# Performance work log

Hardware: AMD Instinct MI355X
Metric: run time of the kernel (lower is better)

The kernel has to match this reference:

```python
import jax, jax.numpy as jnp
import numpy as np

B, H, W, N = 4, 64, 64, 64
NEAR, FAR = 2.0, 6.0
HID = 64


def setup_inputs() -> dict:
    key = jax.random.key(0)
    ks = jax.random.split(key, 6)
    ray_origins = jnp.tile(jnp.array([0.0, 0.0, 4.0], jnp.float32), (B, H, W, 1))
    ray_directions = jax.random.normal(ks[0], (B, H, W, 3), jnp.float32)
    tform_cam2world = jnp.eye(4, dtype=jnp.float32) + 0.1 * jax.random.normal(ks[1], (B, 4, 4), jnp.float32)
    depth_noise = jax.random.uniform(ks[2], (B, H, W, N), jnp.float32)
    u_samples = jax.random.uniform(ks[3], (B, H, W, N), jnp.float32)
    W1 = 0.5 * jax.random.normal(ks[4], (3, HID), jnp.float32)
    b1 = jnp.zeros((HID,), jnp.float32)
    W2 = 0.5 * jax.random.normal(ks[5], (HID, 4), jnp.float32)
    b2 = jnp.zeros((4,), jnp.float32)
    return dict(ray_origins=ray_origins, ray_directions=ray_directions,
                tform_cam2world=tform_cam2world, depth_noise=depth_noise,
                u_samples=u_samples, W1=W1, b1=b1, W2=W2, b2=b2)


def field(pts, W1, b1, W2, b2):
    # tiny radiance-field MLP standing in for the generator's sampler
    h = jax.nn.relu(pts @ W1 + b1)
    out = h @ W2 + b2
    sigma = out[..., 0]
    rgb = jax.nn.sigmoid(out[..., 1:4])
    return sigma, rgb


def compositing_weights(sigma, z_vals):
    # alpha-compositing weights (render_volume_density)
    dists = jnp.concatenate([z_vals[..., 1:] - z_vals[..., :-1],
                             jnp.full_like(z_vals[..., :1], 1e10)], axis=-1)
    alpha = 1.0 - jnp.exp(-jax.nn.relu(sigma) * dists)
    trans = jnp.cumprod(1.0 - alpha + 1e-10, axis=-1)
    trans = jnp.concatenate([jnp.ones_like(trans[..., :1]), trans[..., :-1]], axis=-1)
    return alpha * trans


def sample_pdf(bins, weights, u):
    # bins [R, M+1], weights [R, M], u [R, S] -> samples [R, S]
    pdf = weights / jnp.sum(weights, axis=-1, keepdims=True)
    cdf = jnp.cumsum(pdf, axis=-1)
    cdf = jnp.concatenate([jnp.zeros_like(cdf[..., :1]), cdf], axis=-1)  # [R, M+1]
    inds = jax.vmap(lambda c, uu: jnp.searchsorted(c, uu, side='right'))(cdf, u)
    last = cdf.shape[-1] - 1
    below = jnp.clip(inds - 1, 0, last)
    above = jnp.clip(inds, 0, last)
    cdf_b = jnp.take_along_axis(cdf, below, axis=-1)
    cdf_a = jnp.take_along_axis(cdf, above, axis=-1)
    bin_b = jnp.take_along_axis(bins, below, axis=-1)
    bin_a = jnp.take_along_axis(bins, above, axis=-1)
    denom = cdf_a - cdf_b
    denom = jnp.where(denom < 1e-5, 1.0, denom)
    t = (u - cdf_b) / denom
    return bin_b + t * (bin_a - bin_b)


def reference(ray_origins, ray_directions, tform_cam2world, depth_noise, u_samples, W1, b1, W2, b2):
    rd = ray_directions / jnp.linalg.norm(ray_directions, axis=-1, keepdims=True)
    # stratified coarse samples along each ray
    t = (jnp.arange(N, dtype=jnp.float32) + depth_noise) / N           # [B,H,W,N]
    z_vals = NEAR + (FAR - NEAR) * t
    pts = ray_origins[..., None, :] + rd[..., None, :] * z_vals[..., None]
    sigma, rgb = field(pts, W1, b1, W2, b2)                            # [B,H,W,N], [B,H,W,N,3]

    # --- hierarchical importance sampling (no_grad in original) ---
    w = compositing_weights(sigma, z_vals).reshape(-1, N)              # [R,N]
    pad = jnp.pad(w, ((0, 0), (1, 1)), constant_values=-jnp.inf)
    mx = jnp.maximum(pad[:, :-1], pad[:, 1:])                          # max_pool1d(k=2,s=1,p=1) -> [R,N+1]
    sm = 0.5 * (mx[:, :-1] + mx[:, 1:]) + 0.01                        # avg_pool1d(k=2,s=1)  -> [R,N]
    z_mid = (0.5 * (z_vals[..., 1:] + z_vals[..., :-1])).reshape(-1, N - 1)
    z_samples = sample_pdf(z_mid, sm[:, 1:-1], u_samples.reshape(-1, N))
    z_samples = jax.lax.stop_gradient(z_samples.reshape(B, H, W, N))

    # fine evaluation + merge-sort of coarse/fine samples
    z_all = jnp.concatenate([z_vals, z_samples], axis=-1)              # [B,H,W,2N]
    idx = jnp.argsort(z_all, axis=-1)
    z_sorted = jnp.take_along_axis(z_all, idx, axis=-1)
    pts_f = ray_origins[..., None, :] + rd[..., None, :] * z_samples[..., None]
    sigma_f, rgb_f = field(pts_f, W1, b1, W2, b2)
    sigma_all = jnp.take_along_axis(jnp.concatenate([sigma, sigma_f], axis=-1), idx, axis=-1)
    rgb_cat = jnp.concatenate([rgb, rgb_f], axis=-2)
    rgb_all = jnp.take_along_axis(rgb_cat, jnp.broadcast_to(idx[..., None], idx.shape + (3,)), axis=-2)

    # final alpha compositing
    w_all = compositing_weights(sigma_all, z_sorted)
    rgb_pred = jnp.sum(w_all[..., None] * rgb_all, axis=-2)            # [B,H,W,3]
    depth_pred = jnp.sum(w_all * z_sorted, axis=-1)                    # [B,H,W]
    mask_pred = jnp.sum(w_all, axis=-1)                                # [B,H,W]

    # camera-space depth (invert_space: R_w2c = R^T)
    R_w2c = jnp.swapaxes(tform_cam2world[:, :3, :3], -1, -2)           # [B,3,3]
    view_dir = jnp.einsum('bhwj,bij->bhwi', rd, R_w2c)
    depth_cam = -(view_dir * depth_pred[..., None])[..., -1]
    return rgb_pred, depth_cam, mask_pred
```

## Files before the change

### kernel.cpp

```cpp
#include <hip/hip_runtime.h>
#include <hip/hip_bf16.h>
#include <math.h>

#define Nn    64
#define RPB   2
#define NRAYS 16384
#define NEARV 2.0f
#define FARV  6.0f

typedef __attribute__((ext_vector_type(8))) short bf16x8;
typedef __attribute__((ext_vector_type(4))) float f32x4;
typedef __attribute__((ext_vector_type(2))) float f32x2;

template <int CTRL, int RMASK>
__device__ __forceinline__ float dpp_mv(float x, float ident) {
  return __int_as_float(__builtin_amdgcn_update_dpp(
      __float_as_int(ident), __float_as_int(x), CTRL, RMASK, 0xf, false));
}
__device__ __forceinline__ float shfl_up1(float x) {
  return __int_as_float(__builtin_amdgcn_update_dpp(
      __float_as_int(x), __float_as_int(x), 0x138, 0xf, 0xf, false));
}
__device__ __forceinline__ float shfl_dn1(float x) {
  return __int_as_float(__builtin_amdgcn_update_dpp(
      __float_as_int(x), __float_as_int(x), 0x130, 0xf, 0xf, false));
}
__device__ __forceinline__ float scan_add_dpp(float x) {
  x += dpp_mv<0x111, 0xf>(x, 0.f);
  x += dpp_mv<0x112, 0xf>(x, 0.f);
  x += dpp_mv<0x114, 0xf>(x, 0.f);
  x += dpp_mv<0x118, 0xf>(x, 0.f);
  x += dpp_mv<0x142, 0xa>(x, 0.f);
  x += dpp_mv<0x143, 0xc>(x, 0.f);
  return x;
}
__device__ __forceinline__ float scan_mul_dpp(float x) {
  x *= dpp_mv<0x111, 0xf>(x, 1.f);
  x *= dpp_mv<0x112, 0xf>(x, 1.f);
  x *= dpp_mv<0x114, 0xf>(x, 1.f);
  x *= dpp_mv<0x118, 0xf>(x, 1.f);
  x *= dpp_mv<0x142, 0xa>(x, 1.f);
  x *= dpp_mv<0x143, 0xc>(x, 1.f);
  return x;
}
__device__ __forceinline__ float reduce_add_bcast(float x) {
  x = scan_add_dpp(x);
  return __int_as_float(__builtin_amdgcn_readlane(__float_as_int(x), 63));
}

__device__ __forceinline__ float fast_rcp(float x) { return __builtin_amdgcn_rcpf(x); }
__device__ __forceinline__ float sigmoidf_fast(float x) { return fast_rcp(1.f + __expf(-x)); }

__device__ __forceinline__ short bfhi_bits(float x) { return (short)(__float_as_uint(x) >> 16); }
__device__ __forceinline__ float bfhi_val(float x)  { return __uint_as_float(__float_as_uint(x) & 0xFFFF0000u); }

template <int LEVEL, int D>
__device__ __forceinline__ void bitonic_stage(unsigned& k, int lane) {
  unsigned t;
  if constexpr (D == 32) {
    t = (unsigned)__builtin_amdgcn_ds_bpermute((lane ^ 32) << 2, (int)k);
  } else {
    t = (unsigned)__builtin_amdgcn_ds_swizzle((int)k, (D << 10) | 0x1F);
  }
  const bool bitd = (lane & D) != 0;
  const bool desc = (lane & (1 << LEVEL)) != 0;
  const unsigned mn = (k < t) ? k : t;
  const unsigned mx = (k < t) ? t : k;
  k = (bitd == desc) ? mn : mx;
}
template <int LEVEL, int D>
struct BSort {
  static __device__ __forceinline__ void run(unsigned& k, int lane) {
    bitonic_stage<LEVEL, D>(k, lane);
    if constexpr (D > 1) BSort<LEVEL, D / 2>::run(k, lane);
    else if constexpr (LEVEL < 6) BSort<LEVEL + 1, (1 << LEVEL)>::run(k, lane);
  }
};

template <int D>
__device__ __forceinline__ void merge_stage(unsigned& k, int lane) {
  unsigned t;
  if constexpr (D == 32) {
    t = (unsigned)__builtin_amdgcn_ds_bpermute((lane ^ 32) << 2, (int)k);
  } else {
    t = (unsigned)__builtin_amdgcn_ds_swizzle((int)k, (D << 10) | 0x1F);
  }
  const unsigned mn = (k < t) ? k : t;
  const unsigned mx = (k < t) ? t : k;
  k = ((lane & D) != 0) ? mx : mn;
}
__device__ __forceinline__ void merge64(unsigned& k, int lane) {
  merge_stage<32>(k, lane);
  merge_stage<16>(k, lane);
  merge_stage<8>(k, lane);
  merge_stage<4>(k, lane);
  merge_stage<2>(k, lane);
  merge_stage<1>(k, lane);
}

__device__ __forceinline__ int count_le_f(float arr, float x) {
  int cnt = 0;
#pragma unroll
  for (int step = 32; step >= 1; step >>= 1) {
    const int idx = cnt + step - 1;
    const float v = __shfl(arr, idx, 64);
    if (idx < 63 && v <= x) cnt += step;
  }
  return cnt;
}

template <bool SPLITB>
__device__ __forceinline__ void field_eval(
    float zlane, const f32x2 c0v[2][4], const f32x2 c1v[2][4],
    const bf16x8 aHi[2], const bf16x8 aLo[2],
    float b20, float b21, float b22, float b23,
    int quad, int col, float4* scratch, float o[4]) {
#pragma unroll
  for (int nt = 0; nt < 4; ++nt) {
    f32x4 acc = {0.f, 0.f, 0.f, 0.f};
    const float zm = __shfl(zlane, nt * 16 + col, 64);
    const f32x2 zm2 = {zm, zm};
#pragma unroll
    for (int ks = 0; ks < 2; ++ks) {
      union { bf16x8 v; unsigned u[4]; } Bhi, Blo;
#pragma unroll
      for (int p = 0; p < 4; ++p) {
        f32x2 h = zm2 * c1v[ks][p] + c0v[ks][p];
        h = __builtin_elementwise_max(h, (f32x2){0.f, 0.f});
        if constexpr (SPLITB) {
          union { f32x2 f; unsigned u[2]; } U; U.f = h;
          Bhi.u[p] = __builtin_amdgcn_perm(U.u[1], U.u[0], 0x07060302u);
          union { unsigned u[2]; f32x2 f; } M;
          M.u[0] = U.u[0] & 0xFFFF0000u;
          M.u[1] = U.u[1] & 0xFFFF0000u;
          const f32x2 l = h - M.f;
          union { f32x2 f; unsigned u[2]; } L; L.f = l;
          Blo.u[p] = __builtin_amdgcn_perm(L.u[1], L.u[0], 0x07060302u);
        } else {
          __hip_bfloat162 t = __float22bfloat162_rn(make_float2(h[0], h[1]));
          Bhi.u[p] = *reinterpret_cast<unsigned*>(&t);
        }
      }
      if constexpr (SPLITB) {
        acc = __builtin_amdgcn_mfma_f32_16x16x32_bf16(aHi[ks], Bhi.v, acc, 0, 0, 0);
        acc = __builtin_amdgcn_mfma_f32_16x16x32_bf16(aHi[ks], Blo.v, acc, 0, 0, 0);
        acc = __builtin_amdgcn_mfma_f32_16x16x32_bf16(aLo[ks], Bhi.v, acc, 0, 0, 0);
      } else {
        acc = __builtin_amdgcn_mfma_f32_16x16x32_bf16(aHi[ks], Bhi.v, acc, 0, 0, 0);
        acc = __builtin_amdgcn_mfma_f32_16x16x32_bf16(aLo[ks], Bhi.v, acc, 0, 0, 0);
      }
    }
    if (quad == 0) scratch[nt * 16 + col] = make_float4(acc[0], acc[1], acc[2], acc[3]);
  }
  const float4 r = scratch[(threadIdx.x & 63)];
  o[0] = r.x + b20; o[1] = r.y + b21; o[2] = r.z + b22; o[3] = r.w + b23;
}

__global__ __launch_bounds__(RPB * 64, 4) void nerf_fused(
    const float* __restrict__ ray_o, const float* __restrict__ ray_d,
    const float* __restrict__ tform, const float* __restrict__ noise,
    const float* __restrict__ usmp,  const float* __restrict__ W1,
    const float* __restrict__ b1,    const float* __restrict__ W2,
    const float* __restrict__ b2,    float* __restrict__ out) {
  const int wave = threadIdx.x >> 6;
  const int lane = threadIdx.x & 63;
  const int ray  = blockIdx.x * RPB + wave;
  const int quad = lane >> 4;
  const int col  = lane & 15;

  __shared__ float2 sC [RPB][Nn];
  __shared__ float4 sPk[RPB][2 * Nn];

  const float o0 = ray_o[ray * 3 + 0], o1 = ray_o[ray * 3 + 1], o2 = ray_o[ray * 3 + 2];
  float d0 = ray_d[ray * 3 + 0], d1 = ray_d[ray * 3 + 1], d2 = ray_d[ray * 3 + 2];
  const float rn = __builtin_amdgcn_rsqf(d0 * d0 + d1 * d1 + d2 * d2);
  d0 *= rn; d1 *= rn; d2 *= rn;

  {
    const float w10 = W1[lane], w11 = W1[64 + lane], w12 = W1[128 + lane];
    const float c1 = d0 * w10 + d1 * w11 + d2 * w12;
    const float c0 = o0 * w10 + o1 * w11 + o2 * w12 + b1[lane];
    sC[wave][lane] = make_float2(c0, c1);
  }

  const float nz = noise[ray * Nn + lane];
  const float z  = NEARV + (FARV - NEARV) * ((float)lane + nz) * (1.0f / Nn);
  const unsigned kc = ((__float_as_uint(z) - 0x40000000u) << 7) | (unsigned)lane;

  f32x2 c0v[2][4], c1v[2][4];
#pragma unroll
  for (int ks = 0; ks < 2; ++ks) {
    const float4* cc4 = (const float4*)&sC[wave][0];
    const int base4 = (ks * 32 + quad * 8) >> 1;
#pragma unroll
    for (int jj = 0; jj < 4; ++jj) {
      const float4 v = cc4[base4 + jj];
      c0v[ks][jj] = (f32x2){v.x, v.z};
      c1v[ks][jj] = (f32x2){v.y, v.w};
    }
  }

  bf16x8 aHi[2], aLo[2];
#pragma unroll
  for (int ks = 0; ks < 2; ++ks) {
#pragma unroll
    for (int j = 0; j < 8; ++j) {
      const int k = ks * 32 + quad * 8 + j;
      const float wv  = (col < 4) ? W2[k * 4 + col] : 0.f;
      aHi[ks][j] = bfhi_bits(wv);
      aLo[ks][j] = bfhi_bits(wv - bfhi_val(wv));
    }
  }
  const float b20 = b2[0], b21 = b2[1], b22 = b2[2], b23 = b2[3];
  float4* scratch = &sPk[wave][64];

  float oc[4];
  field_eval<true>(z, c0v, c1v, aHi, aLo, b20, b21, b22, b23, quad, col, scratch, oc);
  const float sig = oc[0];
  const float cr = sigmoidf_fast(oc[1]), cg = sigmoidf_fast(oc[2]), cb = sigmoidf_fast(oc[3]);
  sPk[wave][lane] = make_float4(sig, cr, cg, cb);

  const float zn   = shfl_dn1(z);
  const float dist = (lane == 63) ? 1e10f : (zn - z);
  const float alpha = 1.f - __expf(-fmaxf(sig, 0.f) * dist);
  float cdfreg, binreg;
  {
    const float P  = scan_mul_dpp(1.f - alpha + 1e-10f);
    float Te = shfl_up1(P);
    if (lane == 0) Te = 1.f;
    const float w = alpha * Te;

    const float mxA = fmaxf(shfl_up1(w), w);
    const float mxB = fmaxf(w, shfl_dn1(w));
    const float sm = 0.5f * (mxA + mxB) + 0.01f;

    const float v   = (lane >= 1 && lane <= 62) ? sm : 0.f;
    const float tot = reduce_add_bcast(v);
    const float pdf = v * fast_rcp(tot);
    const float C   = scan_add_dpp(pdf);
    cdfreg = (lane == 0) ? 0.f : C;
    binreg = 0.5f * (z + zn);
  }

  const float u = usmp[ray * Nn + lane];
  const int lo_i = count_le_f(cdfreg, u);
  const int below = lo_i - 1;
  const int above = (lo_i < 63) ? lo_i : 62;
  const float cdfb = __shfl(cdfreg, below, 64);
  const float cdfa = __shfl(cdfreg, above, 64);
  const float binb = __shfl(binreg, below, 64);
  const float bina = __shfl(binreg, above, 64);
  float den = cdfa - cdfb;
  if (den < 1e-5f) den = 1.f;
  const float zs = fmaf((u - cdfb) * fast_rcp(den), bina - binb, binb);

  const unsigned kf = ((__float_as_uint(zs) - 0x40000000u) << 7) | (unsigned)(64 + lane);
  unsigned kfS = kf;
  BSort<1, 1>::run(kfS, lane);

  float of[4];
  field_eval<false>(zs, c0v, c1v, aHi, aLo, b20, b21, b22, b23, quad, col, scratch, of);

  unsigned lok = kc;
  unsigned hik = (unsigned)__builtin_amdgcn_ds_bpermute((63 - lane) << 2, (int)kfS);
  {
    const unsigned mn = (lok < hik) ? lok : hik;
    const unsigned mx = (lok < hik) ? hik : lok;
    lok = mn; hik = mx;
  }
  merge64(lok, lane);
  merge64(hik, lane);

  const float sigF = of[0];
  const float fr = sigmoidf_fast(of[1]), fg = sigmoidf_fast(of[2]), fb = sigmoidf_fast(of[3]);
  sPk[wave][64 + lane] = make_float4(sigF, fr, fg, fb);

  const int a0 = ((2 * lane) & 63) << 2;
  const int a1 = ((2 * lane + 1) & 63) << 2;
  const unsigned l0 = (unsigned)__builtin_amdgcn_ds_bpermute(a0, (int)lok);
  const unsigned h0 = (unsigned)__builtin_amdgcn_ds_bpermute(a0, (int)hik);
  const unsigned l1 = (unsigned)__builtin_amdgcn_ds_bpermute(a1, (int)lok);
  const unsigned h1 = (unsigned)__builtin_amdgcn_ds_bpermute(a1, (int)hik);
  const unsigned k0 = (lane < 32) ? l0 : h0;
  const unsigned k1 = (lane < 32) ? l1 : h1;

  const float z0 = __uint_as_float((k0 >> 7) + 0x40000000u);
  const float z1 = __uint_as_float((k1 >> 7) + 0x40000000u);
  const float4 q0 = sPk[wave][k0 & 127u];
  const float4 q1 = sPk[wave][k1 & 127u];

  const float z2 = shfl_dn1(z0);
  const float dist0 = z1 - z0;
  const float dist1 = (lane == 63) ? 1e10f : (z2 - z1);
  const float al0 = 1.f - __expf(-fmaxf(q0.x, 0.f) * dist0);
  const float al1 = 1.f - __expf(-fmaxf(q1.x, 0.f) * dist1);
  const float aa0 = 1.f - al0 + 1e-10f;
  const float aa1 = 1.f - al1 + 1e-10f;
  const float Pp = scan_mul_dpp(aa0 * aa1);
  float Tp = shfl_up1(Pp);
  if (lane == 0) Tp = 1.f;
  const float w0 = al0 * Tp;
  const float w1 = al1 * Tp * aa0;

  const float accR = reduce_add_bcast(w0 * q0.y + w1 * q1.y);
  const float accG = reduce_add_bcast(w0 * q0.z + w1 * q1.z);
  const float accB = reduce_add_bcast(w0 * q0.w + w1 * q1.w);
  const float accD = reduce_add_bcast(w0 * z0 + w1 * z1);
  const float accM = reduce_add_bcast(w0 + w1);

  if (lane == 0) {
    const float* tf = tform + (ray >> 12) * 16;
    const float vz = d0 * tf[2] + d1 * tf[6] + d2 * tf[10];
    out[ray * 3 + 0]     = accR;
    out[ray * 3 + 1]     = accG;
    out[ray * 3 + 2]     = accB;
    out[NRAYS * 3 + ray] = -vz * accD;
    out[NRAYS * 4 + ray] = accM;
  }
}

extern "C" void kernel_launch(void* const* d_in, const int* in_sizes, int n_in,
                              void* d_out, int out_size, void* d_ws, size_t ws_size,
                              hipStream_t stream) {
  const float* ray_o = (const float*)d_in[0];
  const float* ray_d = (const float*)d_in[1];
  const float* tform = (const float*)d_in[2];
  const float* noise = (const float*)d_in[3];
  const float* usmp  = (const float*)d_in[4];
  const float* W1    = (const float*)d_in[5];
  const float* b1    = (const float*)d_in[6];
  const float* W2    = (const float*)d_in[7];
  const float* b2    = (const float*)d_in[8];
  float* out = (float*)d_out;

  nerf_fused<<<dim3(NRAYS / RPB), RPB * 64, 0, stream>>>(
      ray_o, ray_d, tform, noise, usmp, W1, b1, W2, b2, out);
}
```

Baseline: 101.8 us.

## Process two rays per wavefront to interleave independent dependency chains

Each wave now handles two rays, with per-ray state in arrays and each stage (field eval, scans, sampling, sort/merge, compositing) run for both rays back to back. This gives the scheduler independent instructions to hide latency in the serial DPP scans, shuffles and MFMA chains, and reuses W1/W2 register loads across rays. The grid is halved and launch bounds drop to 2 waves/SIMD, so register pressure and occupancy shift in exchange for ILP.

```diff
diff --git a/kernel.cpp b/kernel.cpp
--- a/kernel.cpp
+++ b/kernel.cpp
@@ -3,7 +3,7 @@
 #include <math.h>
 
 #define Nn    64
-#define RPB   2
+#define WPB   2
 #define NRAYS 16384
 #define NEARV 2.0f
 #define FARV  6.0f
@@ -156,7 +156,7 @@
   o[0] = r.x + b20; o[1] = r.y + b21; o[2] = r.z + b22; o[3] = r.w + b23;
 }
 
-__global__ __launch_bounds__(RPB * 64, 4) void nerf_fused(
+__global__ __launch_bounds__(WPB * 64, 2) void nerf_fused(
     const float* __restrict__ ray_o, const float* __restrict__ ray_d,
     const float* __restrict__ tform, const float* __restrict__ noise,
     const float* __restrict__ usmp,  const float* __restrict__ W1,
@@ -164,39 +164,47 @@
     const float* __restrict__ b2,    float* __restrict__ out) {
   const int wave = threadIdx.x >> 6;
   const int lane = threadIdx.x & 63;
-  const int ray  = blockIdx.x * RPB + wave;
+  const int ray0 = (blockIdx.x * WPB + wave) * 2;
   const int quad = lane >> 4;
   const int col  = lane & 15;
 
-  __shared__ float2 sC [RPB][Nn];
-  __shared__ float4 sPk[RPB][2 * Nn];
-
-  const float o0 = ray_o[ray * 3 + 0], o1 = ray_o[ray * 3 + 1], o2 = ray_o[ray * 3 + 2];
-  float d0 = ray_d[ray * 3 + 0], d1 = ray_d[ray * 3 + 1], d2 = ray_d[ray * 3 + 2];
-  const float rn = __builtin_amdgcn_rsqf(d0 * d0 + d1 * d1 + d2 * d2);
-  d0 *= rn; d1 *= rn; d2 *= rn;
-
-  {
-    const float w10 = W1[lane], w11 = W1[64 + lane], w12 = W1[128 + lane];
-    const float c1 = d0 * w10 + d1 * w11 + d2 * w12;
-    const float c0 = o0 * w10 + o1 * w11 + o2 * w12 + b1[lane];
-    sC[wave][lane] = make_float2(c0, c1);
-  }
-
-  const float nz = noise[ray * Nn + lane];
-  const float z  = NEARV + (FARV - NEARV) * ((float)lane + nz) * (1.0f / Nn);
-  const unsigned kc = ((__float_as_uint(z) - 0x40000000u) << 7) | (unsigned)lane;
-
-  f32x2 c0v[2][4], c1v[2][4];
-#pragma unroll
-  for (int ks = 0; ks < 2; ++ks) {
-    const float4* cc4 = (const float4*)&sC[wave][0];
-    const int base4 = (ks * 32 + quad * 8) >> 1;
-#pragma unroll
-    for (int jj = 0; jj < 4; ++jj) {
-      const float4 v = cc4[base4 + jj];
-      c0v[ks][jj] = (f32x2){v.x, v.z};
-      c1v[ks][jj] = (f32x2){v.y, v.w};
+  __shared__ float2 sC [WPB][2][Nn];
+  __shared__ float4 sPk[WPB][2][2 * Nn];
+
+  const float w10 = W1[lane], w11 = W1[64 + lane], w12 = W1[128 + lane];
+  const float b1v = b1[lane];
+
+  float d0[2], d1[2], d2[2], z[2];
+  unsigned kc[2];
+#pragma unroll
+  for (int r = 0; r < 2; ++r) {
+    const int ray = ray0 + r;
+    const float o0 = ray_o[ray * 3 + 0], o1 = ray_o[ray * 3 + 1], o2 = ray_o[ray * 3 + 2];
+    float dd0 = ray_d[ray * 3 + 0], dd1 = ray_d[ray * 3 + 1], dd2 = ray_d[ray * 3 + 2];
+    const float rn = __builtin_amdgcn_rsqf(dd0 * dd0 + dd1 * dd1 + dd2 * dd2);
+    dd0 *= rn; dd1 *= rn; dd2 *= rn;
+    d0[r] = dd0; d1[r] = dd1; d2[r] = dd2;
+    const float c1 = dd0 * w10 + dd1 * w11 + dd2 * w12;
+    const float c0 = o0 * w10 + o1 * w11 + o2 * w12 + b1v;
+    sC[wave][r][lane] = make_float2(c0, c1);
+    const float nz = noise[ray * Nn + lane];
+    z[r] = NEARV + (FARV - NEARV) * ((float)lane + nz) * (1.0f / Nn);
+    kc[r] = ((__float_as_uint(z[r]) - 0x40000000u) << 7) | (unsigned)lane;
+  }
+
+  f32x2 c0v[2][2][4], c1v[2][2][4];
+#pragma unroll
+  for (int r = 0; r < 2; ++r) {
+    const float4* cc4 = (const float4*)&sC[wave][r][0];
+#pragma unroll
+    for (int ks = 0; ks < 2; ++ks) {
+      const int base4 = (ks * 32 + quad * 8) >> 1;
+#pragma unroll
+      for (int jj = 0; jj < 4; ++jj) {
+        const float4 v = cc4[base4 + jj];
+        c0v[r][ks][jj] = (f32x2){v.x, v.z};
+        c1v[r][ks][jj] = (f32x2){v.y, v.w};
+      }
     }
   }
 
@@ -212,110 +220,132 @@
     }
   }
   const float b20 = b2[0], b21 = b2[1], b22 = b2[2], b23 = b2[3];
-  float4* scratch = &sPk[wave][64];
-
-  float oc[4];
-  field_eval<true>(z, c0v, c1v, aHi, aLo, b20, b21, b22, b23, quad, col, scratch, oc);
-  const float sig = oc[0];
-  const float cr = sigmoidf_fast(oc[1]), cg = sigmoidf_fast(oc[2]), cb = sigmoidf_fast(oc[3]);
-  sPk[wave][lane] = make_float4(sig, cr, cg, cb);
-
-  const float zn   = shfl_dn1(z);
-  const float dist = (lane == 63) ? 1e10f : (zn - z);
-  const float alpha = 1.f - __expf(-fmaxf(sig, 0.f) * dist);
-  float cdfreg, binreg;
-  {
+  float4* scr0 = &sPk[wave][0][64];
+  float4* scr1 = &sPk[wave][1][64];
+
+  float oc[2][4];
+  field_eval<true>(z[0], c0v[0], c1v[0], aHi, aLo, b20, b21, b22, b23, quad, col, scr0, oc[0]);
+  field_eval<true>(z[1], c0v[1], c1v[1], aHi, aLo, b20, b21, b22, b23, quad, col, scr1, oc[1]);
+
+  float sig[2];
+#pragma unroll
+  for (int r = 0; r < 2; ++r) {
+    sig[r] = oc[r][0];
+    sPk[wave][r][lane] = make_float4(sig[r], sigmoidf_fast(oc[r][1]),
+                                     sigmoidf_fast(oc[r][2]), sigmoidf_fast(oc[r][3]));
+  }
+
+  float cdfreg[2], binreg[2];
+#pragma unroll
+  for (int r = 0; r < 2; ++r) {
+    const float zn   = shfl_dn1(z[r]);
+    const float dist = (lane == 63) ? 1e10f : (zn - z[r]);
+    const float alpha = 1.f - __expf(-fmaxf(sig[r], 0.f) * dist);
     const float P  = scan_mul_dpp(1.f - alpha + 1e-10f);
     float Te = shfl_up1(P);
     if (lane == 0) Te = 1.f;
     const float w = alpha * Te;
-
     const float mxA = fmaxf(shfl_up1(w), w);
     const float mxB = fmaxf(w, shfl_dn1(w));
     const float sm = 0.5f * (mxA + mxB) + 0.01f;
-
     const float v   = (lane >= 1 && lane <= 62) ? sm : 0.f;
     const float tot = reduce_add_bcast(v);
     const float pdf = v * fast_rcp(tot);
     const float C   = scan_add_dpp(pdf);
-    cdfreg = (lane == 0) ? 0.f : C;
-    binreg = 0.5f * (z + zn);
-  }
-
-  const float u = usmp[ray * Nn + lane];
-  const int lo_i = count_le_f(cdfreg, u);
-  const int below = lo_i - 1;
-  const int above = (lo_i < 63) ? lo_i : 62;
-  const float cdfb = __shfl(cdfreg, below, 64);
-  const float cdfa = __shfl(cdfreg, above, 64);
-  const float binb = __shfl(binreg, below, 64);
-  const float bina = __shfl(binreg, above, 64);
-  float den = cdfa - cdfb;
-  if (den < 1e-5f) den = 1.f;
-  const float zs = fmaf((u - cdfb) * fast_rcp(den), bina - binb, binb);
-
-  const unsigned kf = ((__float_as_uint(zs) - 0x40000000u) << 7) | (unsigned)(64 + lane);
-  unsigned kfS = kf;
-  BSort<1, 1>::run(kfS, lane);
-
-  float of[4];
-  field_eval<false>(zs, c0v, c1v, aHi, aLo, b20, b21, b22, b23, quad, col, scratch, of);
-
-  unsigned lok = kc;
-  unsigned hik = (unsigned)__builtin_amdgcn_ds_bpermute((63 - lane) << 2, (int)kfS);
-  {
-    const unsigned mn = (lok < hik) ? lok : hik;
-    const unsigned mx = (lok < hik) ? hik : lok;
-    lok = mn; hik = mx;
-  }
-  merge64(lok, lane);
-  merge64(hik, lane);
-
-  const float sigF = of[0];
-  const float fr = sigmoidf_fast(of[1]), fg = sigmoidf_fast(of[2]), fb = sigmoidf_fast(of[3]);
-  sPk[wave][64 + lane] = make_float4(sigF, fr, fg, fb);
+    cdfreg[r] = (lane == 0) ? 0.f : C;
+    binreg[r] = 0.5f * (z[r] + zn);
+  }
+
+  float zs[2];
+#pragma unroll
+  for (int r = 0; r < 2; ++r) {
+    const float u = usmp[(ray0 + r) * Nn + lane];
+    const int lo_i = count_le_f(cdfreg[r], u);
+    const int below = lo_i - 1;
+    const int above = (lo_i < 63) ? lo_i : 62;
+    const float cdfb = __shfl(cdfreg[r], below, 64);
+    const float cdfa = __shfl(cdfreg[r], above, 64);
+    const float binb = __shfl(binreg[r], below, 64);
+    const float bina = __shfl(binreg[r], above, 64);
+    float den = cdfa - cdfb;
+    if (den < 1e-5f) den = 1.f;
+    zs[r] = fmaf((u - cdfb) * fast_rcp(den), bina - binb, binb);
+  }
+
+  unsigned kfS[2];
+#pragma unroll
+  for (int r = 0; r < 2; ++r) {
+    kfS[r] = ((__float_as_uint(zs[r]) - 0x40000000u) << 7) | (unsigned)(64 + lane);
+    BSort<1, 1>::run(kfS[r], lane);
+  }
+
+  float of[2][4];
+  field_eval<false>(zs[0], c0v[0], c1v[0], aHi, aLo, b20, b21, b22, b23, quad, col, scr0, of[0]);
+  field_eval<false>(zs[1], c0v[1], c1v[1], aHi, aLo, b20, b21, b22, b23, quad, col, scr1, of[1]);
+
+  unsigned lok[2], hik[2];
+#pragma unroll
+  for (int r = 0; r < 2; ++r) {
+    unsigned lo = kc[r];
+    unsigned hi = (unsigned)__builtin_amdgcn_ds_bpermute((63 - lane) << 2, (int)kfS[r]);
+    const unsigned mn = (lo < hi) ? lo : hi;
+    const unsigned mx = (lo < hi) ? hi : lo;
+    lo = mn; hi = mx;
+    merge64(lo, lane);
+    merge64(hi, lane);
+    lok[r] = lo; hik[r] = hi;
+  }
+
+#pragma unroll
+  for (int r = 0; r < 2; ++r)
+    sPk[wave][r][64 + lane] = make_float4(of[r][0], sigmoidf_fast(of[r][1]),
+                                          sigmoidf_fast(of[r][2]), sigmoidf_fast(of[r][3]));
 
   const int a0 = ((2 * lane) & 63) << 2;
   const int a1 = ((2 * lane + 1) & 63) << 2;
-  const unsigned l0 = (unsigned)__builtin_amdgcn_ds_bpermute(a0, (int)lok);
-  const unsigned h0 = (unsigned)__builtin_amdgcn_ds_bpermute(a0, (int)hik);
-  const unsigned l1 = (unsigned)__builtin_amdgcn_ds_bpermute(a1, (int)lok);
-  const unsigned h1 = (unsigned)__builtin_amdgcn_ds_bpermute(a1, (int)hik);
-  const unsigned k0 = (lane < 32) ? l0 : h0;
-  const unsigned k1 = (lane < 32) ? l1 : h1;
-
-  const float z0 = __uint_as_float((k0 >> 7) + 0x40000000u);
-  const float z1 = __uint_as_float((k1 >> 7) + 0x40000000u);
-  const float4 q0 = sPk[wave][k0 & 127u];
-  const float4 q1 = sPk[wave][k1 & 127u];
-
-  const float z2 = shfl_dn1(z0);
-  const float dist0 = z1 - z0;
-  const float dist1 = (lane == 63) ? 1e10f : (z2 - z1);
-  const float al0 = 1.f - __expf(-fmaxf(q0.x, 0.f) * dist0);
-  const float al1 = 1.f - __expf(-fmaxf(q1.x, 0.f) * dist1);
-  const float aa0 = 1.f - al0 + 1e-10f;
-  const float aa1 = 1.f - al1 + 1e-10f;
-  const float Pp = scan_mul_dpp(aa0 * aa1);
-  float Tp = shfl_up1(Pp);
-  if (lane == 0) Tp = 1.f;
-  const float w0 = al0 * Tp;
-  const float w1 = al1 * Tp * aa0;
-
-  const float accR = reduce_add_bcast(w0 * q0.y + w1 * q1.y);
-  const float accG = reduce_add_bcast(w0 * q0.z + w1 * q1.z);
-  const float accB = reduce_add_bcast(w0 * q0.w + w1 * q1.w);
-  const float accD = reduce_add_bcast(w0 * z0 + w1 * z1);
-  const float accM = reduce_add_bcast(w0 + w1);
-
-  if (lane == 0) {
-    const float* tf = tform + (ray >> 12) * 16;
-    const float vz = d0 * tf[2] + d1 * tf[6] + d2 * tf[10];
-    out[ray * 3 + 0]     = accR;
-    out[ray * 3 + 1]     = accG;
-    out[ray * 3 + 2]     = accB;
-    out[NRAYS * 3 + ray] = -vz * accD;
-    out[NRAYS * 4 + ray] = accM;
+#pragma unroll
+  for (int r = 0; r < 2; ++r) {
+    const unsigned l0 = (unsigned)__builtin_amdgcn_ds_bpermute(a0, (int)lok[r]);
+    const unsigned h0 = (unsigned)__builtin_amdgcn_ds_bpermute(a0, (int)hik[r]);
+    const unsigned l1 = (unsigned)__builtin_amdgcn_ds_bpermute(a1, (int)lok[r]);
+    const unsigned h1 = (unsigned)__builtin_amdgcn_ds_bpermute(a1, (int)hik[r]);
+    const unsigned k0 = (lane < 32) ? l0 : h0;
+    const unsigned k1 = (lane < 32) ? l1 : h1;
+
+    const float z0 = __uint_as_float((k0 >> 7) + 0x40000000u);
+    const float z1 = __uint_as_float((k1 >> 7) + 0x40000000u);
+    const float4 q0 = sPk[wave][r][k0 & 127u];
+    const float4 q1 = sPk[wave][r][k1 & 127u];
+
+    const float z2 = shfl_dn1(z0);
+    const float dist0 = z1 - z0;
+    const float dist1 = (lane == 63) ? 1e10f : (z2 - z1);
+    const float al0 = 1.f - __expf(-fmaxf(q0.x, 0.f) * dist0);
+    const float al1 = 1.f - __expf(-fmaxf(q1.x, 0.f) * dist1);
+    const float aa0 = 1.f - al0 + 1e-10f;
+    const float aa1 = 1.f - al1 + 1e-10f;
+    const float Pp = scan_mul_dpp(aa0 * aa1);
+    float Tp = shfl_up1(Pp);
+    if (lane == 0) Tp = 1.f;
+    const float w0 = al0 * Tp;
+    const float w1 = al1 * Tp * aa0;
+
+    const float accR = reduce_add_bcast(w0 * q0.y + w1 * q1.y);
+    const float accG = reduce_add_bcast(w0 * q0.z + w1 * q1.z);
+    const float accB = reduce_add_bcast(w0 * q0.w + w1 * q1.w);
+    const float accD = reduce_add_bcast(w0 * z0 + w1 * z1);
+    const float accM = reduce_add_bcast(w0 + w1);
+
+    if (lane == 0) {
+      const int ray = ray0 + r;
+      const float* tf = tform + (ray >> 12) * 16;
+      const float vz = d0[r] * tf[2] + d1[r] * tf[6] + d2[r] * tf[10];
+      out[ray * 3 + 0]     = accR;
+      out[ray * 3 + 1]     = accG;
+      out[ray * 3 + 2]     = accB;
+      out[NRAYS * 3 + ray] = -vz * accD;
+      out[NRAYS * 4 + ray] = accM;
+    }
   }
 }
 
@@ -333,6 +363,6 @@
   const float* b2    = (const float*)d_in[8];
   float* out = (float*)d_out;
 
-  nerf_fused<<<dim3(NRAYS / RPB), RPB * 64, 0, stream>>>(
+  nerf_fused<<<dim3(NRAYS / (2 * WPB)), WPB * 64, 0, stream>>>(
       ray_o, ray_d, tform, noise, usmp, W1, b1, W2, b2, out);
 }
```

New measurement: 104.0 us. +2.1%, slower.
